# Kernel tuning notes

Measured on AMD Instinct MI355X. Metric: run time of the kernel, lower is better.

The kernel has to match this reference:

```python
import jax, jax.numpy as jnp
import numpy as np

D_MODEL = 1024
NUM_HEADS = 16
D_K = D_MODEL // NUM_HEADS
NEG_INF = -1e9


def setup_inputs() -> dict:
    key = jax.random.key(0)
    ks = jax.random.split(key, 12)
    B, S = 2, 2048
    Q = jax.random.normal(ks[0], (B, S, D_MODEL), jnp.float32)
    K = jax.random.normal(ks[1], (B, S, D_MODEL), jnp.float32)
    V = jax.random.normal(ks[2], (B, S, D_MODEL), jnp.float32)
    mask = jax.random.randint(ks[3], (B, 1, 1, S), 0, 2, jnp.int32)
    scale = 1.0 / np.sqrt(D_MODEL)
    WQ = jax.random.normal(ks[4], (D_MODEL, D_MODEL), jnp.float32) * scale
    bQ = jnp.zeros((D_MODEL,), jnp.float32)
    WK = jax.random.normal(ks[5], (D_MODEL, D_MODEL), jnp.float32) * scale
    bK = jnp.zeros((D_MODEL,), jnp.float32)
    WV = jax.random.normal(ks[6], (D_MODEL, D_MODEL), jnp.float32) * scale
    bV = jnp.zeros((D_MODEL,), jnp.float32)
    WO = jax.random.normal(ks[7], (D_MODEL, D_MODEL), jnp.float32) * scale
    bO = jnp.zeros((D_MODEL,), jnp.float32)
    return {"Q": Q, "K": K, "V": V, "mask": mask,
            "WQ": WQ, "bQ": bQ, "WK": WK, "bK": bK,
            "WV": WV, "bV": bV, "WO": WO, "bO": bO}


def _split_heads(x):
    # (B, S, d_model) -> (B, H, S, d_k)
    B, S, _ = x.shape
    return x.reshape(B, S, NUM_HEADS, D_K).transpose(0, 2, 1, 3)


def reference(Q, K, V, mask, WQ, bQ, WK, bK, WV, bV, WO, bO):
    B, Sq, _ = Q.shape
    q = _split_heads(Q @ WQ + bQ)   # (B, H, Sq, d_k)
    k = _split_heads(K @ WK + bK)   # (B, H, Sk, d_k)
    v = _split_heads(V @ WV + bV)   # (B, H, Sk, d_v)
    scores = jnp.einsum('bhqd,bhkd->bhqk', q, k) / jnp.sqrt(jnp.float32(D_K))
    scores = jnp.where(mask == 0, jnp.float32(NEG_INF), scores)
    attention = jax.nn.softmax(scores, axis=-1)         # (B, H, Sq, Sk)
    context = jnp.einsum('bhqk,bhkd->bhqd', attention, v)
    context = context.transpose(0, 2, 1, 3).reshape(B, Sq, D_MODEL)
    output = context @ WO + bO
    return (output, attention)
```

## Files before the change

### kernel.cpp

```cpp
#include <hip/hip_runtime.h>

typedef __attribute__((ext_vector_type(8))) __bf16 bf16x8;
typedef __attribute__((ext_vector_type(4))) __bf16 bf16x4;
typedef __attribute__((ext_vector_type(4))) float f32x4;

#define DEVFN static __device__ __forceinline__

#if __has_builtin(__builtin_amdgcn_exp2f)
#define EXP2(x) __builtin_amdgcn_exp2f(x)
#else
#define EXP2(x) exp2f(x)
#endif

DEVFN f32x4 mfma16(bf16x8 a, bf16x8 b, f32x4 c) {
  return __builtin_amdgcn_mfma_f32_16x16x32_bf16(a, b, c, 0, 0, 0);
}

DEVFN void gload16(const void* g, void* l) {
  __builtin_amdgcn_global_load_lds((const __attribute__((address_space(1))) void*)g,
                                   (__attribute__((address_space(3))) void*)l, 16, 0, 0);
}

__global__ __launch_bounds__(256) void transW4(const float* __restrict__ w0,
                                               const float* __restrict__ w1,
                                               const float* __restrict__ w2,
                                               const float* __restrict__ w3,
                                               unsigned short* __restrict__ obase) {
  __shared__ float t[64][65];
  const float* W = blockIdx.z == 0 ? w0 : blockIdx.z == 1 ? w1 : blockIdx.z == 2 ? w2 : w3;
  unsigned short* Wt = obase + ((size_t)blockIdx.z << 20);
  int k0 = blockIdx.x * 64, n0 = blockIdx.y * 64;
  int tid = threadIdx.x;
#pragma unroll
  for (int it = 0; it < 4; ++it) {
    int r = it * 16 + (tid >> 4);
    int c = (tid & 15) * 4;
    float4 v = *(const float4*)(W + (size_t)(k0 + r) * 1024 + n0 + c);
    t[r][c] = v.x; t[r][c + 1] = v.y; t[r][c + 2] = v.z; t[r][c + 3] = v.w;
  }
  __syncthreads();
#pragma unroll
  for (int it = 0; it < 2; ++it) {
    int nl = it * 32 + (tid >> 3);
    int kc = tid & 7;
    bf16x8 o;
#pragma unroll
    for (int j = 0; j < 8; ++j) o[j] = (__bf16)t[kc * 8 + j][nl];
    int n = n0 + nl;
    char* dst = (char*)Wt + (size_t)n * 2048 + (k0 << 1) + ((kc ^ (n & 7)) << 4);
    *(bf16x8*)dst = o;
  }
}

struct GArg {
  const void* A;
  const unsigned short* Bt;
  const float* bias;
  void* out;
  float scale;
};

template <int BM, int BN, int WR, int WC, int AF32, int EPI, int OCC>
__global__ __launch_bounds__(256, OCC) void gemm_t(GArg g0, GArg g1, GArg g2) {
  GArg g = blockIdx.z == 0 ? g0 : blockIdx.z == 1 ? g1 : g2;
  constexpr int MT = BM / WR / 16, NT = BN / WC / 16;
  constexpr int AB = AF32 ? 4 : 2;
  __shared__ char lA[BM * 64 * AB];
  __shared__ char lB[BN * 64 * 2];
  int tid = threadIdx.x, wave = tid >> 6, lane = tid & 63;
  int hi = lane >> 4, lo = lane & 15;
  int m0 = blockIdx.x * BM, n0 = blockIdx.y * BN;
  int wr = wave / WC, wc = wave % WC;
  f32x4 acc[MT][NT];
#pragma unroll
  for (int mt = 0; mt < MT; ++mt)
#pragma unroll
    for (int nt = 0; nt < NT; ++nt) acc[mt][nt] = (f32x4){0.f, 0.f, 0.f, 0.f};

  for (int k0 = 0; k0 < 1024; k0 += 64) {
    if (AF32) {
#pragma unroll
      for (int i = 0; i < BM / 16; ++i) {
        int off = i * 4096 + tid * 16;
        int row = off >> 8, b = off & 255;
        gload16((const char*)g.A + (size_t)(m0 + row) * 4096 + (k0 << 2)
                    + (b ^ ((row & 7) << 4)),
                lA + i * 4096 + wave * 1024);
      }
    } else {
#pragma unroll
      for (int i = 0; i < BM / 32; ++i) {
        int off = i * 4096 + tid * 16;
        int row = off >> 7, b = off & 127;
        gload16((const char*)g.A + (size_t)(m0 + row) * 2048 + (k0 << 1) + b,
                lA + i * 4096 + wave * 1024);
      }
    }
#pragma unroll
    for (int i = 0; i < BN / 32; ++i) {
      int off = i * 4096 + tid * 16;
      int row = off >> 7, b = off & 127;
      gload16((const char*)g.Bt + (size_t)(n0 + row) * 2048 + (k0 << 1) + b,
              lB + i * 4096 + wave * 1024);
    }
    __syncthreads();
#pragma unroll
    for (int kk = 0; kk < 2; ++kk) {
      bf16x8 af[MT], bfr[NT];
#pragma unroll
      for (int mt = 0; mt < MT; ++mt) {
        int row = wr * (BM / WR) + mt * 16 + lo;
        if (AF32) {
          int base = (row << 8) + ((kk << 7) + (hi << 5));
          int sw = (row & 7) << 4;
          f32x4 a0 = *(const f32x4*)(lA + ((base) ^ sw));
          f32x4 a1 = *(const f32x4*)(lA + ((base + 16) ^ sw));
          bf16x8 v;
#pragma unroll
          for (int j = 0; j < 4; ++j) { v[j] = (__bf16)a0[j]; v[4 + j] = (__bf16)a1[j]; }
          af[mt] = v;
        } else {
          int ob = (row << 7) + ((((kk << 2) + hi) << 4) ^ ((row & 7) << 4));
          af[mt] = *(const bf16x8*)(lA + ob);
        }
      }
#pragma unroll
      for (int nt = 0; nt < NT; ++nt) {
        int row = wc * (BN / WC) + nt * 16 + lo;
        int ob = (row << 7) + ((((kk << 2) + hi) << 4) ^ ((row & 7) << 4));
        bfr[nt] = *(const bf16x8*)(lB + ob);
      }
#pragma unroll
      for (int mt = 0; mt < MT; ++mt)
#pragma unroll
        for (int nt = 0; nt < NT; ++nt)
          acc[mt][nt] = mfma16(af[mt], bfr[nt], acc[mt][nt]);
    }
    __syncthreads();
  }

#pragma unroll
  for (int mt = 0; mt < MT; ++mt) {
#pragma unroll
    for (int nt = 0; nt < NT; ++nt) {
      int col = n0 + wc * (BN / WC) + nt * 16 + lo;
      float bs = g.bias[col];
      int row0 = m0 + wr * (BM / WR) + mt * 16 + (hi << 2);
      float vj[4];
#pragma unroll
      for (int j = 0; j < 4; ++j) vj[j] = (acc[mt][nt][j] + bs) * g.scale;
      if (EPI == 1) {
#pragma unroll
        for (int j = 0; j < 4; ++j)
          ((float*)g.out)[(size_t)(row0 + j) * 1024 + col] = vj[j];
      } else if (blockIdx.z == 2) {
        int d = col & 63;
        int bh = (row0 >> 11) * 16 + (col >> 6);
        int s = row0 & 2047;
        bf16x4 o;
#pragma unroll
        for (int j = 0; j < 4; ++j) o[j] = (__bf16)vj[j];
        char* p = (char*)g.out + ((size_t)bh << 18) + (size_t)d * 4096
                  + (s >> 6) * 128 + (((((s & 63) >> 3) ^ (d & 7)) << 4))
                  + ((s & 7) << 1);
        *(bf16x4*)p = o;
      } else {
#pragma unroll
        for (int j = 0; j < 4; ++j) {
          int srow = row0 + j;
          size_t hb = ((size_t)((srow >> 11) * 16 + (col >> 6))) << 18;
          int ib = ((srow & 2047) << 7) + (((col & 63) << 1) ^ ((srow & 7) << 4));
          *(__bf16*)((char*)g.out + hb + ib) = (__bf16)vj[j];
        }
      }
    }
  }
}

__global__ __launch_bounds__(512, 4) void attn_k(
    const unsigned short* __restrict__ qh, const unsigned short* __restrict__ kh,
    const unsigned short* __restrict__ vt, const int* __restrict__ mask,
    float* __restrict__ attn, unsigned short* __restrict__ ctx) {
  constexpr int S = 2048;
  __shared__ unsigned short ktl[64 * 64];
  __shared__ unsigned short vtl[64 * 64];
  __shared__ unsigned long long mkb[32];
  __shared__ float pf[8][16 * 68];

  int tid = threadIdx.x, wave = tid >> 6, lane = tid & 63;
  int hi = lane >> 4, lo = lane & 15;
  int f = blockIdx.y * 16 + blockIdx.x;
  int xcd = f & 7, slot = f >> 3;
  int bh = xcd * 4 + (slot & 3);
  int qb = slot >> 2;
  int b = bh >> 4, h = bh & 15;
  const char* khead = (const char*)kh + ((size_t)bh << 18);
  const char* qhead = (const char*)qh + ((size_t)bh << 18);
  const char* vhead = (const char*)vt + ((size_t)bh << 18);

  for (int it = 0; it < 4; ++it) {
    unsigned long long bal = __ballot(mask[b * S + it * 512 + tid] != 0);
    if (lane == 0) mkb[it * 8 + wave] = bal;
  }
  __syncthreads();

  int q0 = qb * 128 + wave * 16;
  bf16x8 qf[2];
  {
    int row = q0 + lo;
#pragma unroll
    for (int kk = 0; kk < 2; ++kk) {
      int ib = (row << 7) + ((((kk << 2) + hi) << 4) ^ ((row & 7) << 4));
      qf[kk] = *(const bf16x8*)(qhead + ib);
    }
  }

  float lsum[4] = {0.f, 0.f, 0.f, 0.f};

  gload16(khead + tid * 16, (char*)ktl + wave * 1024);
  for (int kt = 0; kt < 32; ++kt) {
    const char* cb = (kt & 1) ? (const char*)vtl : (const char*)ktl;
    char* nb = (kt & 1) ? (char*)ktl : (char*)vtl;
    if (kt < 31) {
      gload16(khead + (size_t)(kt + 1) * 8192 + tid * 16, nb + wave * 1024);
      asm volatile("s_waitcnt vmcnt(1)" ::: "memory");
    } else {
      asm volatile("s_waitcnt vmcnt(0)" ::: "memory");
    }
    __builtin_amdgcn_sched_barrier(0);
    __builtin_amdgcn_s_barrier();
    unsigned long long mw = mkb[kt];
    __builtin_amdgcn_s_setprio(1);
#pragma unroll
    for (int nt = 0; nt < 4; ++nt) {
      int r = nt * 16 + lo;
      f32x4 a = {0.f, 0.f, 0.f, 0.f};
#pragma unroll
      for (int kk = 0; kk < 2; ++kk) {
        int ob = (r << 7) + ((((kk << 2) + hi) << 4) ^ ((r & 7) << 4));
        a = mfma16(qf[kk], *(const bf16x8*)(cb + ob), a);
      }
      bool ok = (mw >> r) & 1ull;
#pragma unroll
      for (int j = 0; j < 4; ++j) lsum[j] += ok ? EXP2(a[j]) : 0.f;
    }
    __builtin_amdgcn_s_setprio(0);
    __builtin_amdgcn_sched_barrier(0);
    __builtin_amdgcn_s_barrier();
    __builtin_amdgcn_sched_barrier(0);
  }

  float rcp[4];
#pragma unroll
  for (int j = 0; j < 4; ++j) {
    float s = lsum[j];
    s += __shfl_xor(s, 1); s += __shfl_xor(s, 2);
    s += __shfl_xor(s, 4); s += __shfl_xor(s, 8);
    rcp[j] = s > 0.f ? 1.0f / s : 0.f;
  }

  f32x4 cacc[4];
#pragma unroll
  for (int nt = 0; nt < 4; ++nt) cacc[nt] = (f32x4){0.f, 0.f, 0.f, 0.f};

  float* arow = attn + (size_t)bh * S * S;
  float* pfw = pf[wave];

  for (int kt = 0; kt < 32; ++kt) {
    gload16(khead + (size_t)kt * 8192 + tid * 16, (char*)ktl + wave * 1024);
    {
      int d = tid >> 3, x = (tid & 7) * 16;
      gload16(vhead + (size_t)d * 4096 + kt * 128 + x, (char*)vtl + wave * 1024);
    }
    __syncthreads();
    unsigned long long mw = mkb[kt];
    __builtin_amdgcn_s_setprio(1);
#pragma unroll
    for (int nt = 0; nt < 4; ++nt) {
      int r = nt * 16 + lo;
      f32x4 a = {0.f, 0.f, 0.f, 0.f};
#pragma unroll
      for (int kk = 0; kk < 2; ++kk) {
        int ob = (r << 7) + ((((kk << 2) + hi) << 4) ^ ((r & 7) << 4));
        a = mfma16(qf[kk], *(const bf16x8*)((const char*)ktl + ob), a);
      }
      bool ok = (mw >> r) & 1ull;
#pragma unroll
      for (int j = 0; j < 4; ++j) {
        float pn = ok ? EXP2(a[j]) * rcp[j] : 0.f;
        pfw[((hi << 2) + j) * 68 + r] = pn;
      }
    }
    __builtin_amdgcn_s_setprio(0);
    {
      int rsub = lane >> 4;
      int cb = (lane & 15) << 2;
#pragma unroll
      for (int s = 0; s < 4; ++s) {
        int row = s * 4 + rsub;
        f32x4 v = *(const f32x4*)&pfw[row * 68 + cb];
        __builtin_nontemporal_store(
            v, (f32x4*)(arow + (size_t)(q0 + row) * S + kt * 64 + cb));
      }
    }
    __builtin_amdgcn_s_setprio(1);
#pragma unroll
    for (int c = 0; c < 2; ++c) {
      f32x4 p0 = *(const f32x4*)&pfw[lo * 68 + c * 32 + hi * 8];
      f32x4 p1 = *(const f32x4*)&pfw[lo * 68 + c * 32 + hi * 8 + 4];
      bf16x8 pa;
#pragma unroll
      for (int i = 0; i < 4; ++i) { pa[i] = (__bf16)p0[i]; pa[4 + i] = (__bf16)p1[i]; }
#pragma unroll
      for (int nt = 0; nt < 4; ++nt) {
        int d = nt * 16 + lo;
        int ob = (d << 7) + ((((c << 2) + hi) << 4) ^ ((d & 7) << 4));
        cacc[nt] = mfma16(pa, *(const bf16x8*)((const char*)vtl + ob), cacc[nt]);
      }
    }
    __builtin_amdgcn_s_setprio(0);
    __syncthreads();
  }

#pragma unroll
  for (int nt = 0; nt < 4; ++nt) {
#pragma unroll
    for (int j = 0; j < 4; ++j) {
      int s = q0 + (hi << 2) + j;
      int mrow = b * S + s;
      int n = h * 64 + nt * 16 + lo;
      int ib = (n << 1) ^ ((mrow & 7) << 4);
      *(__bf16*)((char*)ctx + (size_t)mrow * 2048 + ib) = (__bf16)cacc[nt][j];
    }
  }
}

extern "C" void kernel_launch(void* const* d_in, const int* in_sizes, int n_in,
                              void* d_out, int out_size, void* d_ws, size_t ws_size,
                              hipStream_t stream) {
  const float* Q  = (const float*)d_in[0];
  const float* K  = (const float*)d_in[1];
  const float* V  = (const float*)d_in[2];
  const int* mask = (const int*)d_in[3];
  const float* WQ = (const float*)d_in[4];
  const float* bQ = (const float*)d_in[5];
  const float* WK = (const float*)d_in[6];
  const float* bK = (const float*)d_in[7];
  const float* WV = (const float*)d_in[8];
  const float* bV = (const float*)d_in[9];
  const float* WO = (const float*)d_in[10];
  const float* bO = (const float*)d_in[11];

  char* ws = (char*)d_ws;
  const size_t M1 = 1ull << 20;
  unsigned short* WQt = (unsigned short*)(ws + 0 * M1);
  unsigned short* WKt = (unsigned short*)(ws + 2 * M1);
  unsigned short* WVt = (unsigned short*)(ws + 4 * M1);
  unsigned short* WOt = (unsigned short*)(ws + 6 * M1);
  unsigned short* qh  = (unsigned short*)(ws + 8 * M1);
  unsigned short* kh  = (unsigned short*)(ws + 16 * M1);
  unsigned short* vt  = (unsigned short*)(ws + 24 * M1);
  unsigned short* ctx = (unsigned short*)(ws + 32 * M1);

  float* outF = (float*)d_out;
  float* attn = (float*)d_out + 4194304;

  const float qscale = 0.125f * 1.44269504088896340736f;

  transW4<<<dim3(16, 16, 4), dim3(256), 0, stream>>>(WQ, WK, WV, WO, WQt);

  GArg aq{Q, WQt, bQ, qh, qscale};
  GArg ak{K, WKt, bK, kh, 1.f};
  GArg av{V, WVt, bV, vt, 1.f};
  gemm_t<128, 128, 2, 2, 1, 0, 3><<<dim3(32, 8, 3), dim3(256), 0, stream>>>(aq, ak, av);

  attn_k<<<dim3(16, 32), dim3(512), 0, stream>>>(qh, kh, vt, mask, attn, ctx);

  GArg ao{ctx, WOt, bO, outF, 1.f};
  gemm_t<64, 128, 1, 4, 0, 1, 2><<<dim3(64, 8, 1), dim3(256), 0, stream>>>(ao, ao, ao);
}
```

Measured before the change: 225.2 us.

## Process two key tiles per barrier in attention passes with larger LDS buffers

The attention kernel now handles two 64-key tiles per iteration in both passes, using four LDS tile buffers instead of two. This halves the number of block-wide barriers and load waits per row block. Pass one double-buffers pairs of tiles, while pass two loads two K and two V tiles and then processes both before syncing. The extra 16KB of LDS may reduce occupancy, and pass two still waits with no prefetch overlap.

```diff
diff --git a/kernel.cpp b/kernel.cpp
--- a/kernel.cpp
+++ b/kernel.cpp
@@ -182,8 +182,7 @@
     const unsigned short* __restrict__ vt, const int* __restrict__ mask,
     float* __restrict__ attn, unsigned short* __restrict__ ctx) {
   constexpr int S = 2048;
-  __shared__ unsigned short ktl[64 * 64];
-  __shared__ unsigned short vtl[64 * 64];
+  __shared__ unsigned short buf[4][64 * 64];
   __shared__ unsigned long long mkb[32];
   __shared__ float pf[8][16 * 68];
 
@@ -217,32 +216,40 @@
 
   float lsum[4] = {0.f, 0.f, 0.f, 0.f};
 
-  gload16(khead + tid * 16, (char*)ktl + wave * 1024);
-  for (int kt = 0; kt < 32; ++kt) {
-    const char* cb = (kt & 1) ? (const char*)vtl : (const char*)ktl;
-    char* nb = (kt & 1) ? (char*)ktl : (char*)vtl;
-    if (kt < 31) {
-      gload16(khead + (size_t)(kt + 1) * 8192 + tid * 16, nb + wave * 1024);
-      asm volatile("s_waitcnt vmcnt(1)" ::: "memory");
+#pragma unroll
+  for (int i = 0; i < 2; ++i)
+    gload16(khead + (size_t)i * 8192 + tid * 16, (char*)buf[i] + wave * 1024);
+  for (int t = 0; t < 16; ++t) {
+    int p = (t & 1) << 1;
+    if (t < 15) {
+#pragma unroll
+      for (int i = 0; i < 2; ++i)
+        gload16(khead + (size_t)(2 * t + 2 + i) * 8192 + tid * 16,
+                (char*)buf[(p ^ 2) + i] + wave * 1024);
+      asm volatile("s_waitcnt vmcnt(2)" ::: "memory");
     } else {
       asm volatile("s_waitcnt vmcnt(0)" ::: "memory");
     }
     __builtin_amdgcn_sched_barrier(0);
     __builtin_amdgcn_s_barrier();
-    unsigned long long mw = mkb[kt];
     __builtin_amdgcn_s_setprio(1);
 #pragma unroll
-    for (int nt = 0; nt < 4; ++nt) {
-      int r = nt * 16 + lo;
-      f32x4 a = {0.f, 0.f, 0.f, 0.f};
-#pragma unroll
-      for (int kk = 0; kk < 2; ++kk) {
-        int ob = (r << 7) + ((((kk << 2) + hi) << 4) ^ ((r & 7) << 4));
-        a = mfma16(qf[kk], *(const bf16x8*)(cb + ob), a);
-      }
-      bool ok = (mw >> r) & 1ull;
-#pragma unroll
-      for (int j = 0; j < 4; ++j) lsum[j] += ok ? EXP2(a[j]) : 0.f;
+    for (int half = 0; half < 2; ++half) {
+      unsigned long long mw = mkb[2 * t + half];
+      const char* cb = (const char*)buf[p + half];
+#pragma unroll
+      for (int nt = 0; nt < 4; ++nt) {
+        int r = nt * 16 + lo;
+        f32x4 a = {0.f, 0.f, 0.f, 0.f};
+#pragma unroll
+        for (int kk = 0; kk < 2; ++kk) {
+          int ob = (r << 7) + ((((kk << 2) + hi) << 4) ^ ((r & 7) << 4));
+          a = mfma16(qf[kk], *(const bf16x8*)(cb + ob), a);
+        }
+        bool ok = (mw >> r) & 1ull;
+#pragma unroll
+        for (int j = 0; j < 4; ++j) lsum[j] += ok ? EXP2(a[j]) : 0.f;
+      }
     }
     __builtin_amdgcn_s_setprio(0);
     __builtin_amdgcn_sched_barrier(0);
@@ -266,60 +273,78 @@
   float* arow = attn + (size_t)bh * S * S;
   float* pfw = pf[wave];
 
-  for (int kt = 0; kt < 32; ++kt) {
-    gload16(khead + (size_t)kt * 8192 + tid * 16, (char*)ktl + wave * 1024);
+  for (int t = 0; t < 16; ++t) {
+#pragma unroll
+    for (int i = 0; i < 2; ++i)
+      gload16(khead + (size_t)(2 * t + i) * 8192 + tid * 16,
+              (char*)buf[i] + wave * 1024);
     {
       int d = tid >> 3, x = (tid & 7) * 16;
-      gload16(vhead + (size_t)d * 4096 + kt * 128 + x, (char*)vtl + wave * 1024);
-    }
-    __syncthreads();
-    unsigned long long mw = mkb[kt];
-    __builtin_amdgcn_s_setprio(1);
-#pragma unroll
-    for (int nt = 0; nt < 4; ++nt) {
-      int r = nt * 16 + lo;
-      f32x4 a = {0.f, 0.f, 0.f, 0.f};
-#pragma unroll
-      for (int kk = 0; kk < 2; ++kk) {
-        int ob = (r << 7) + ((((kk << 2) + hi) << 4) ^ ((r & 7) << 4));
-        a = mfma16(qf[kk], *(const bf16x8*)((const char*)ktl + ob), a);
-      }
-      bool ok = (mw >> r) & 1ull;
-#pragma unroll
-      for (int j = 0; j < 4; ++j) {
-        float pn = ok ? EXP2(a[j]) * rcp[j] : 0.f;
-        pfw[((hi << 2) + j) * 68 + r] = pn;
-      }
-    }
-    __builtin_amdgcn_s_setprio(0);
-    {
-      int rsub = lane >> 4;
-      int cb = (lane & 15) << 2;
-#pragma unroll
-      for (int s = 0; s < 4; ++s) {
-        int row = s * 4 + rsub;
-        f32x4 v = *(const f32x4*)&pfw[row * 68 + cb];
-        __builtin_nontemporal_store(
-            v, (f32x4*)(arow + (size_t)(q0 + row) * S + kt * 64 + cb));
-      }
-    }
-    __builtin_amdgcn_s_setprio(1);
-#pragma unroll
-    for (int c = 0; c < 2; ++c) {
-      f32x4 p0 = *(const f32x4*)&pfw[lo * 68 + c * 32 + hi * 8];
-      f32x4 p1 = *(const f32x4*)&pfw[lo * 68 + c * 32 + hi * 8 + 4];
-      bf16x8 pa;
-#pragma unroll
-      for (int i = 0; i < 4; ++i) { pa[i] = (__bf16)p0[i]; pa[4 + i] = (__bf16)p1[i]; }
+#pragma unroll
+      for (int i = 0; i < 2; ++i)
+        gload16(vhead + (size_t)d * 4096 + (2 * t + i) * 128 + x,
+                (char*)buf[2 + i] + wave * 1024);
+    }
+    asm volatile("s_waitcnt vmcnt(0)" ::: "memory");
+    __builtin_amdgcn_sched_barrier(0);
+    __builtin_amdgcn_s_barrier();
+    __builtin_amdgcn_sched_barrier(0);
+
+#pragma unroll
+    for (int half = 0; half < 2; ++half) {
+      int kt = 2 * t + half;
+      unsigned long long mw = mkb[kt];
+      const char* kc = (const char*)buf[half];
+      const char* vc = (const char*)buf[2 + half];
+      __builtin_amdgcn_s_setprio(1);
 #pragma unroll
       for (int nt = 0; nt < 4; ++nt) {
-        int d = nt * 16 + lo;
-        int ob = (d << 7) + ((((c << 2) + hi) << 4) ^ ((d & 7) << 4));
-        cacc[nt] = mfma16(pa, *(const bf16x8*)((const char*)vtl + ob), cacc[nt]);
-      }
-    }
-    __builtin_amdgcn_s_setprio(0);
-    __syncthreads();
+        int r = nt * 16 + lo;
+        f32x4 a = {0.f, 0.f, 0.f, 0.f};
+#pragma unroll
+        for (int kk = 0; kk < 2; ++kk) {
+          int ob = (r << 7) + ((((kk << 2) + hi) << 4) ^ ((r & 7) << 4));
+          a = mfma16(qf[kk], *(const bf16x8*)(kc + ob), a);
+        }
+        bool ok = (mw >> r) & 1ull;
+#pragma unroll
+        for (int j = 0; j < 4; ++j) {
+          float pn = ok ? EXP2(a[j]) * rcp[j] : 0.f;
+          pfw[((hi << 2) + j) * 68 + r] = pn;
+        }
+      }
+      __builtin_amdgcn_s_setprio(0);
+      {
+        int rsub = lane >> 4;
+        int cb = (lane & 15) << 2;
+#pragma unroll
+        for (int s = 0; s < 4; ++s) {
+          int row = s * 4 + rsub;
+          f32x4 v = *(const f32x4*)&pfw[row * 68 + cb];
+          __builtin_nontemporal_store(
+              v, (f32x4*)(arow + (size_t)(q0 + row) * S + kt * 64 + cb));
+        }
+      }
+      __builtin_amdgcn_s_setprio(1);
+#pragma unroll
+      for (int c = 0; c < 2; ++c) {
+        f32x4 p0 = *(const f32x4*)&pfw[lo * 68 + c * 32 + hi * 8];
+        f32x4 p1 = *(const f32x4*)&pfw[lo * 68 + c * 32 + hi * 8 + 4];
+        bf16x8 pa;
+#pragma unroll
+        for (int i = 0; i < 4; ++i) { pa[i] = (__bf16)p0[i]; pa[4 + i] = (__bf16)p1[i]; }
+#pragma unroll
+        for (int nt = 0; nt < 4; ++nt) {
+          int d = nt * 16 + lo;
+          int ob = (d << 7) + ((((c << 2) + hi) << 4) ^ ((d & 7) << 4));
+          cacc[nt] = mfma16(pa, *(const bf16x8*)(vc + ob), cacc[nt]);
+        }
+      }
+      __builtin_amdgcn_s_setprio(0);
+    }
+    __builtin_amdgcn_sched_barrier(0);
+    __builtin_amdgcn_s_barrier();
+    __builtin_amdgcn_sched_barrier(0);
   }
 
 #pragma unroll
```

New measurement: 239.2 us. 6.2% more time.
